# Performance work log

Hardware: AMD Instinct MI355X
Metric: run time of the kernel (lower is better)

## Reference

```python
import jax, jax.numpy as jnp
import numpy as np

M = 5            # Anderson memory
LAM = 1e-4       # Tikhonov regularization on Gram matrix
MAX_ITER = 50
TOL = 0.01
BETA = 1.0
BSZ, DIM = 64, 4096


def f_layer(z, x, W, b):
    # canonical DEQ cell: contraction so the fixed point exists
    return jnp.tanh(z @ W + x + b)


def anderson(f, x0, m=M, lam=LAM, max_iter=MAX_ITER, tol=TOL, beta=BETA):
    """Anderson acceleration; faithful port of DEQFixedPoint.anderson.
    Variable history length n=min(k,m) is handled by masking so the whole
    loop is jit-compatible (lax.while_loop with early stop on tol)."""
    bsz = x0.shape[0]
    d = int(np.prod(x0.shape[1:]))
    ff = lambda v: f(v.reshape(x0.shape)).reshape(bsz, d)
    x0f = x0.reshape(bsz, d)

    X = jnp.zeros((bsz, m, d), x0.dtype)
    F = jnp.zeros((bsz, m, d), x0.dtype)
    F0 = ff(x0f)
    F1 = ff(F0)
    X = X.at[:, 0].set(x0f).at[:, 1].set(F0)
    F = F.at[:, 0].set(F0).at[:, 1].set(F1)

    y = jnp.zeros((bsz, m + 1, 1), x0.dtype).at[:, 0, 0].set(1.0)
    eye_m = jnp.eye(m, dtype=x0.dtype)

    def cond(state):
        _, _, k, res = state
        return (k < max_iter) & (res >= tol)

    def body(state):
        X, F, k, res = state
        n = jnp.minimum(k, m)
        mask = (jnp.arange(m) < n).astype(x0.dtype)          # active history slots
        G = (F - X) * mask[None, :, None]                     # (bsz, m, d)
        GG = jnp.einsum('bmd,bnd->bmn', G, G)                 # small 5x5 Gram
        # masked (n+1)x(n+1) subproblem embedded in (m+1)x(m+1): inactive
        # rows become identity rows with zero rhs -> alpha_i = 0 for i >= n,
        # exactly matching torch's solve on the leading (n+1) block.
        Hin = (GG + lam * eye_m) * (mask[:, None] * mask[None, :]) + jnp.diag(1.0 - mask)
        H = jnp.zeros((bsz, m + 1, m + 1), x0.dtype)
        H = H.at[:, 0, 1:].set(mask).at[:, 1:, 0].set(mask).at[:, 1:, 1:].set(Hin)
        alpha = jnp.linalg.solve(H, y)[:, 1:, 0]              # (bsz, m)
        Xk = beta * jnp.einsum('bm,bmd->bd', alpha, F) + (1.0 - beta) * jnp.einsum('bm,bmd->bd', alpha, X)
        Fk = ff(Xk)
        idx = k % m
        Xn = X.at[:, idx].set(Xk)
        Fn = F.at[:, idx].set(Fk)
        r = jnp.linalg.norm(Fk - Xk) / (1e-5 + jnp.linalg.norm(Fk))
        return Xn, Fn, k + 1, r

    init = (X, F, jnp.array(2, jnp.int32), jnp.array(jnp.inf, x0.dtype))
    X, F, k, res = jax.lax.while_loop(cond, body, init)
    idx = (k - 1) % m  # k was incremented after the last executed iteration
    return X[:, idx].reshape(x0.shape)


def setup_inputs():
    key = jax.random.key(0)
    kx, kw, kb = jax.random.split(key, 3)
    x = jax.random.normal(kx, (BSZ, DIM), jnp.float32)
    # spectral norm of W ~ 2 * 0.4 = 0.8 -> contraction through tanh
    W = jax.random.normal(kw, (DIM, DIM), jnp.float32) * (0.4 / np.sqrt(DIM))
    b = jax.random.normal(kb, (DIM,), jnp.float32) * 0.1
    return {"x": x, "W": W, "b": b}


def reference(x, W, b):
    # forward: solve z* = f(z*, x) with no grad, then one grad-carrying f step
    zstar = anderson(lambda z: f_layer(z, x, W, b), jnp.zeros_like(x))
    return f_layer(zstar, x, W, b)
```

## Files before the change

### kernel.cpp

```cpp
#include <hip/hip_runtime.h>

#define NBLK 256
#define GBLK 128
#define NTHR 1024
#define BSZ 64
#define DIM 4096
#define MEM 5
#define MAXIT 50
#define TOL_ 0.01f
#define LAM_ 1e-4f

#define X_OFF 0
#define F_OFF (BSZ * MEM * DIM)
#define Z_OFF (2 * BSZ * MEM * DIM)
#define RP_OFF (Z_OFF + BSZ * DIM)
#define BAR_OFF (RP_OFF + 512)
#define FP32_WS_FLOATS (RP_OFF + 1024)
#define ZF_BYTE ((size_t)(RP_OFF + 1024) * 4)
#define WF_BYTE (ZF_BYTE + (size_t)BSZ * DIM * 2)
#define WS_NEED (WF_BYTE + (size_t)DIM * DIM * 2)

typedef __attribute__((ext_vector_type(8))) _Float16 half8v;
typedef __attribute__((ext_vector_type(4))) float f32x4;

__device__ __forceinline__ unsigned short f2h(float f) {
    _Float16 h = (_Float16)f;
    unsigned short u;
    __builtin_memcpy(&u, &h, 2);
    return u;
}

__device__ __forceinline__ void gridbar(unsigned int* flags, unsigned int* go,
                                        unsigned int e)
{
    __syncthreads();
    const int tid = threadIdx.x;
    if (blockIdx.x == 0) {
        if (tid == 0) {
            __builtin_amdgcn_fence(__ATOMIC_RELEASE, "agent");
            __hip_atomic_store(&flags[0], e, __ATOMIC_RELAXED,
                               __HIP_MEMORY_SCOPE_AGENT);
        }
        if (tid < NBLK) {
            while (__hip_atomic_load(&flags[tid], __ATOMIC_RELAXED,
                                     __HIP_MEMORY_SCOPE_AGENT) < e)
                __builtin_amdgcn_s_sleep(1);
        }
        __syncthreads();
        if (tid == 0)
            __builtin_amdgcn_fence(__ATOMIC_ACQUIRE, "agent");
        __syncthreads();
        if (tid < 8)
            __hip_atomic_store(&go[tid << 5], e, __ATOMIC_RELAXED,
                               __HIP_MEMORY_SCOPE_AGENT);
    } else {
        if (tid == 0) {
            __builtin_amdgcn_fence(__ATOMIC_RELEASE, "agent");
            __hip_atomic_store(&flags[blockIdx.x], e, __ATOMIC_RELAXED,
                               __HIP_MEMORY_SCOPE_AGENT);
            while (__hip_atomic_load(&go[(blockIdx.x >> 5) << 5], __ATOMIC_RELAXED,
                                     __HIP_MEMORY_SCOPE_AGENT) < e)
                __builtin_amdgcn_s_sleep(1);
            __builtin_amdgcn_fence(__ATOMIC_ACQUIRE, "agent");
        }
    }
    __syncthreads();
}

__device__ void convert_w(const float* __restrict__ W, unsigned short* __restrict__ Wf,
                          float* smem)
{
    const int tid = threadIdx.x;
    const int blk = blockIdx.x;
    const int jc = blk << 4;
    for (int sc = 0; sc < 8; ++sc) {
        __syncthreads();
        #pragma unroll
        for (int h = 0; h < 2; ++h) {
            int rrow = (tid >> 2) + (h << 8);
            int seg = tid & 3;
            float4 v = *(const float4*)&W[(size_t)((sc << 9) + rrow) * DIM + jc + (seg << 2)];
            float* dst = smem + rrow * 17 + (seg << 2);
            dst[0] = v.x; dst[1] = v.y; dst[2] = v.z; dst[3] = v.w;
        }
        __syncthreads();
        unsigned int* of = (unsigned int*)(Wf + ((size_t)blk * 128 + sc * 16) * 512);
        #pragma unroll
        for (int it = 0; it < 4; ++it) {
            int o = tid + (it << 10);
            int ksl = o >> 8, ln = (o >> 2) & 63, ep = o & 3;
            int kl = (ksl << 5) + ((ln >> 4) << 3) + (ep << 1);
            float w0 = smem[kl * 17 + (ln & 15)];
            float w1 = smem[(kl + 1) * 17 + (ln & 15)];
            of[o] = (unsigned int)f2h(w0) | ((unsigned int)f2h(w1) << 16);
        }
    }
    __syncthreads();
}

__device__ __forceinline__ void gemm_tanh_mfma(
    int idx, const float* __restrict__ x, const float* __restrict__ bias,
    const unsigned short* __restrict__ Zf, const unsigned short* __restrict__ Wf,
    float* __restrict__ Z, float* __restrict__ Fs, float* __restrict__ rp, float* smem)
{
    const int tid = threadIdx.x;
    const int cb = blockIdx.x;
    const int lane = tid & 63;
    const int w = tid >> 6;
    const int r0 = lane & 15;
    const int kg = lane >> 4;
    f32x4 acc[4][2] = {};

    const unsigned short* b0 = Wf + (size_t)(cb * 2) * 65536;
    const unsigned short* b1 = Wf + (size_t)(cb * 2 + 1) * 65536;
    const int ksbase = w << 3;

    #pragma unroll 2
    for (int s = 0; s < 8; ++s) {
        const int ks = ksbase + s;
        const size_t bo = ((size_t)ks << 9) + (lane << 3);
        half8v B0 = *(const half8v*)(b0 + bo);
        half8v B1 = *(const half8v*)(b1 + bo);
        const int kbase = (ks << 5) + (kg << 3);
        #pragma unroll
        for (int m = 0; m < 4; ++m) {
            const size_t ao = (size_t)((m << 4) + r0) * DIM + kbase;
            half8v Ah = *(const half8v*)(Zf + ao);
            acc[m][0] = __builtin_amdgcn_mfma_f32_16x16x32_f16(Ah, B0, acc[m][0], 0, 0, 0);
            acc[m][1] = __builtin_amdgcn_mfma_f32_16x16x32_f16(Ah, B1, acc[m][1], 0, 0, 0);
        }
    }
    const int row = tid >> 4, cc = tid & 15;
    const int m_o = row >> 4, rl = row & 15;
    const int lsrc = cc + ((rl >> 2) << 4), reg = rl & 3;
    float sum0 = 0.f, sum1 = 0.f;
    #pragma unroll
    for (int rnd = 0; rnd < 4; ++rnd) {
        __syncthreads();
        if ((w >> 2) == rnd) {
            float* sec = smem + (w & 3) * 2052;
            #pragma unroll
            for (int m = 0; m < 4; ++m) {
                *(f32x4*)(sec + ((m * 2 + 0) << 8) + (lane << 2)) = acc[m][0];
                *(f32x4*)(sec + ((m * 2 + 1) << 8) + (lane << 2)) = acc[m][1];
            }
        }
        __syncthreads();
        #pragma unroll
        for (int p = 0; p < 4; ++p) {
            sum0 += smem[p * 2052 + ((m_o * 2 + 0) << 8) + (lsrc << 2) + reg];
            sum1 += smem[p * 2052 + ((m_o * 2 + 1) << 8) + (lsrc << 2) + reg];
        }
    }
    const int j0 = (cb << 5) + cc;
    const int j1 = j0 + 16;
    float fz0 = tanhf(sum0 + x[(row << 12) + j0] + bias[j0]);
    float fz1 = tanhf(sum1 + x[(row << 12) + j1] + bias[j1]);
    Fs[(row * MEM + idx) * DIM + j0] = fz0;
    Fs[(row * MEM + idx) * DIM + j1] = fz1;
    float d0 = fz0 - Z[(row << 12) + j0];
    float d1 = fz1 - Z[(row << 12) + j1];
    float lnum = d0 * d0 + d1 * d1;
    float lden = fz0 * fz0 + fz1 * fz1;
    #pragma unroll
    for (int off = 1; off < 64; off <<= 1) {
        lnum += __shfl_xor(lnum, off, 64);
        lden += __shfl_xor(lden, off, 64);
    }
    if (lane == 0) { smem[8448 + w] = lnum; smem[8480 + w] = lden; }
    __syncthreads();
    if (tid == 0) {
        float a = 0.f, b2 = 0.f;
        #pragma unroll
        for (int i = 0; i < 16; ++i) { a += smem[8448 + i]; b2 += smem[8480 + i]; }
        rp[cb] = a;
        rp[NBLK + cb] = b2;
    }
}

__device__ __forceinline__ void gemm_tanh_fp32(
    int idx, const float* __restrict__ x, const float* __restrict__ W,
    const float* __restrict__ bias, float* __restrict__ wsf, float* smem)
{
    const int tid = threadIdx.x;
    const int blk = blockIdx.x;
    const int lane = tid & 63;
    const int w = tid >> 6;
    const int r = w >> 2;
    const int q = w & 3;
    const int jcq = (blk << 4) + (q << 2);
    float* Z = wsf + Z_OFF;
    float* Fs = wsf + F_OFF;
    float* rp = wsf + RP_OFF;

    float acc0 = 0.f, acc1 = 0.f, acc2 = 0.f, acc3 = 0.f;
    const int lx = lane & 15;
    const float* inrow = smem + (r << 12) + (lane << 6);
    const int srow = tid >> 4;
    const int sg = tid & 15;

    for (int step = 0; step < 16; ++step) {
        #pragma unroll
        for (int i = 0; i < 4; ++i) {
            float4 v = *(const float4*)&Z[srow * DIM + (i << 10) + (step << 6) + (sg << 2)];
            *(float4*)&smem[(i << 12) + (srow << 6) + ((sg ^ (srow & 15)) << 2)] = v;
        }
        __syncthreads();
        const float* wbase = W + (size_t)((r << 10) + (step << 6)) * DIM + jcq;
        #pragma unroll 2
        for (int s = 0; s < 16; ++s) {
            float4 in4 = *(const float4*)&inrow[(s ^ lx) << 2];
            const float* wr = wbase + (size_t)(s << 2) * DIM;
            #pragma unroll
            for (int t = 0; t < 4; ++t) {
                float iv = (t == 0) ? in4.x : (t == 1) ? in4.y : (t == 2) ? in4.z : in4.w;
                float4 wq = *(const float4*)(wr + (size_t)t * DIM);
                acc0 = fmaf(iv, wq.x, acc0);
                acc1 = fmaf(iv, wq.y, acc1);
                acc2 = fmaf(iv, wq.z, acc2);
                acc3 = fmaf(iv, wq.w, acc3);
            }
        }
        __syncthreads();
    }
    {
        float* rrow = smem + r * 1088 + lane * 17 + (q << 2);
        rrow[0] = acc0; rrow[1] = acc1; rrow[2] = acc2; rrow[3] = acc3;
    }
    __syncthreads();
    const int row = tid >> 4, cc = tid & 15;
    const int boff = row * 17 + cc;
    float sum = smem[boff] + smem[1088 + boff] + smem[2176 + boff] + smem[3264 + boff];
    const int j = (blk << 4) + cc;
    float fz = tanhf(sum + x[(row << 12) + j] + bias[j]);
    Fs[(row * MEM + idx) * DIM + j] = fz;
    float d = fz - Z[(row << 12) + j];
    float lnum = d * d, lden = fz * fz;
    #pragma unroll
    for (int off = 1; off < 64; off <<= 1) {
        lnum += __shfl_xor(lnum, off, 64);
        lden += __shfl_xor(lden, off, 64);
    }
    if (lane == 0) { smem[8448 + w] = lnum; smem[8480 + w] = lden; }
    __syncthreads();
    if (tid == 0) {
        float a = 0.f, b2 = 0.f;
        for (int i = 0; i < 16; ++i) { a += smem[8448 + i]; b2 += smem[8480 + i]; }
        rp[blk] = a;
        rp[NBLK + blk] = b2;
    }
}

__device__ __forceinline__ float phase_res(const float* __restrict__ rp, float* smem)
{
    const int tid = threadIdx.x;
    const int lane = tid & 63, w = tid >> 6;
    float a = (tid < NBLK) ? rp[tid] : 0.f;
    float b = (tid < NBLK) ? rp[NBLK + tid] : 0.f;
    #pragma unroll
    for (int off = 1; off < 64; off <<= 1) {
        a += __shfl_xor(a, off, 64);
        b += __shfl_xor(b, off, 64);
    }
    if (lane == 0) { smem[w] = a; smem[16 + w] = b; }
    __syncthreads();
    if (tid == 0) {
        float sa = 0.f, sb = 0.f;
        for (int i = 0; i < 16; ++i) { sa += smem[i]; sb += smem[16 + i]; }
        smem[32] = sqrtf(sa) / (1e-5f + sqrtf(sb));
    }
    __syncthreads();
    float res = smem[32];
    __syncthreads();
    return res;
}

template <bool F16>
__device__ void gram_solve_combine(int b, int n, int idx, float* __restrict__ wsf,
                                   unsigned short* __restrict__ Zf, float* smem)
{
    const int tid = threadIdx.x;
    const int lane = tid & 63, w = tid >> 6;
    float* Xs = wsf + X_OFF;
    float* Fs = wsf + F_OFF;
    float* Z = wsf + Z_OFF;
    const int j4 = tid << 2;

    float fv[MEM][4];
    float g[MEM][4];
    #pragma unroll
    for (int i = 0; i < MEM; ++i) {
        float4 f4 = *(const float4*)&Fs[(b * MEM + i) * DIM + j4];
        float4 xv = *(const float4*)&Xs[(b * MEM + i) * DIM + j4];
        fv[i][0] = f4.x; fv[i][1] = f4.y; fv[i][2] = f4.z; fv[i][3] = f4.w;
        bool act = (i < n);
        g[i][0] = act ? (f4.x - xv.x) : 0.f;
        g[i][1] = act ? (f4.y - xv.y) : 0.f;
        g[i][2] = act ? (f4.z - xv.z) : 0.f;
        g[i][3] = act ? (f4.w - xv.w) : 0.f;
    }
    float gg[15];
    {
        int p = 0;
        #pragma unroll
        for (int i = 0; i < MEM; ++i)
            #pragma unroll
            for (int qq = i; qq < MEM; ++qq) {
                float s = 0.f;
                #pragma unroll
                for (int c = 0; c < 4; ++c) s = fmaf(g[i][c], g[qq][c], s);
                gg[p++] = s;
            }
    }
    #pragma unroll
    for (int off = 1; off < 64; off <<= 1)
        #pragma unroll
        for (int p = 0; p < 15; ++p) gg[p] += __shfl_xor(gg[p], off, 64);
    if (lane == 0) {
        #pragma unroll
        for (int p = 0; p < 15; ++p) smem[p * 16 + w] = gg[p];
    }
    __syncthreads();
    if (tid == 0) {
        float G[MEM][MEM];
        int p = 0;
        for (int i = 0; i < MEM; ++i)
            for (int qq = i; qq < MEM; ++qq) {
                float v = 0.f;
                for (int ww = 0; ww < 16; ++ww) v += smem[p * 16 + ww];
                G[i][qq] = v; G[qq][i] = v; ++p;
            }
        float H[6][6], yv[6];
        for (int i = 0; i < 6; ++i) yv[i] = (i == 0) ? 1.f : 0.f;
        H[0][0] = 0.f;
        for (int i = 0; i < MEM; ++i) {
            float mi = (i < n) ? 1.f : 0.f;
            H[0][1 + i] = mi;
            H[1 + i][0] = mi;
        }
        for (int i = 0; i < MEM; ++i)
            for (int qq = 0; qq < MEM; ++qq) {
                float v;
                if (i < n && qq < n) v = G[i][qq] + ((i == qq) ? LAM_ : 0.f);
                else v = (i == qq) ? 1.f : 0.f;
                H[1 + i][1 + qq] = v;
            }
        for (int col = 0; col < 6; ++col) {
            int piv = col;
            float mv = fabsf(H[col][col]);
            for (int rr = col + 1; rr < 6; ++rr) {
                float av = fabsf(H[rr][col]);
                if (av > mv) { mv = av; piv = rr; }
            }
            if (piv != col) {
                for (int c2 = 0; c2 < 6; ++c2) { float tv = H[col][c2]; H[col][c2] = H[piv][c2]; H[piv][c2] = tv; }
                float tv = yv[col]; yv[col] = yv[piv]; yv[piv] = tv;
            }
            float pv = H[col][col];
            for (int rr = col + 1; rr < 6; ++rr) {
                float f = H[rr][col] / pv;
                H[rr][col] = 0.f;
                for (int c2 = col + 1; c2 < 6; ++c2) H[rr][c2] -= f * H[col][c2];
                yv[rr] -= f * yv[col];
            }
        }
        float sol[6];
        for (int col = 5; col >= 0; --col) {
            float s = yv[col];
            for (int c2 = col + 1; c2 < 6; ++c2) s -= H[col][c2] * sol[c2];
            sol[col] = s / H[col][col];
        }
        for (int i = 0; i < MEM; ++i) smem[240 + i] = sol[1 + i];
    }
    __syncthreads();
    float al[MEM];
    #pragma unroll
    for (int i = 0; i < MEM; ++i) al[i] = smem[240 + i];
    float4 zf = {0.f, 0.f, 0.f, 0.f};
    #pragma unroll
    for (int i = 0; i < MEM; ++i) {
        zf.x = fmaf(al[i], fv[i][0], zf.x);
        zf.y = fmaf(al[i], fv[i][1], zf.y);
        zf.z = fmaf(al[i], fv[i][2], zf.z);
        zf.w = fmaf(al[i], fv[i][3], zf.w);
    }
    *(float4*)&Z[(b << 12) + j4] = zf;
    *(float4*)&Xs[(b * MEM + idx) * DIM + j4] = zf;
    if constexpr (F16) {
        unsigned int* z16 = (unsigned int*)(Zf + ((size_t)b << 12) + j4);
        z16[0] = (unsigned int)f2h(zf.x) | ((unsigned int)f2h(zf.y) << 16);
        z16[1] = (unsigned int)f2h(zf.z) | ((unsigned int)f2h(zf.w) << 16);
    }
}

template <bool F16>
__global__ __launch_bounds__(NTHR, 4)
void deq_anderson(const float* __restrict__ x, const float* __restrict__ W,
                  const float* __restrict__ bias, float* __restrict__ out,
                  char* __restrict__ ws)
{
    __shared__ __align__(16) float smem[16384];
    float* wsf = (float*)ws;
    unsigned int* flags = (unsigned int*)(wsf + BAR_OFF);
    unsigned int* go = flags + 256;
    unsigned short* Zf = (unsigned short*)(ws + ZF_BYTE);
    unsigned short* Wf = (unsigned short*)(ws + WF_BYTE);
    const int tid = threadIdx.x;
    const int blk = blockIdx.x;
    const int e = blk * NTHR + tid;
    const int b = e >> 12, j = e & (DIM - 1);
    float* Xs = wsf + X_OFF;
    float* Fs = wsf + F_OFF;
    float* Z = wsf + Z_OFF;
    float* rp = wsf + RP_OFF;
    unsigned int ep = 1;

    {
        float f0 = tanhf(x[e] + bias[j]);
        #pragma unroll
        for (int i = 0; i < MEM; ++i) {
            Xs[(b * MEM + i) * DIM + j] = (i == 1) ? f0 : 0.f;
            Fs[(b * MEM + i) * DIM + j] = (i == 0) ? f0 : 0.f;
        }
        Z[e] = f0;
        if constexpr (F16) Zf[e] = f2h(f0);
    }
    if constexpr (F16) convert_w(W, Wf, smem);
    gridbar(flags, go, ep++);
    if constexpr (F16) {
        if (blk < GBLK)
            gemm_tanh_mfma(1, x, bias, Zf, Wf, Z, Fs, rp, smem);
        else if (tid == 0) { rp[blk] = 0.f; rp[NBLK + blk] = 0.f; }
    } else {
        gemm_tanh_fp32(1, x, W, bias, wsf, smem);
    }
    gridbar(flags, go, ep++);

    int kend = MAXIT;
    for (int k = 2; k < MAXIT; ++k) {
        float res = phase_res(rp, smem);
        if (k > 2 && res < TOL_) { kend = k; break; }
        const int n = (k < MEM) ? k : MEM;
        const int idx = k % MEM;
        if (blk < BSZ) gram_solve_combine<F16>(blk, n, idx, wsf, Zf, smem);
        gridbar(flags, go, ep++);
        if constexpr (F16) {
            if (blk < GBLK)
                gemm_tanh_mfma(idx, x, bias, Zf, Wf, Z, Fs, rp, smem);
        } else {
            gemm_tanh_fp32(idx, x, W, bias, wsf, smem);
        }
        gridbar(flags, go, ep++);
    }

    const int fidx = (kend - 1) % MEM;
    out[e] = Fs[(b * MEM + fidx) * DIM + j];
}

extern "C" void kernel_launch(void* const* d_in, const int* in_sizes, int n_in,
                              void* d_out, int out_size, void* d_ws, size_t ws_size,
                              hipStream_t stream)
{
    (void)in_sizes; (void)n_in; (void)out_size;
    if (ws_size < (size_t)FP32_WS_FLOATS * sizeof(float)) return;
    const float* x = (const float*)d_in[0];
    const float* W = (const float*)d_in[1];
    const float* b = (const float*)d_in[2];
    float* out = (float*)d_out;
    char* ws = (char*)d_ws;
    hipMemsetAsync(ws + (size_t)BAR_OFF * 4, 0, 2048, stream);
    void* args[] = {(void*)&x, (void*)&W, (void*)&b, (void*)&out, (void*)&ws};
    const void* fn = (ws_size >= WS_NEED)
                         ? reinterpret_cast<const void*>(&deq_anderson<true>)
                         : reinterpret_cast<const void*>(&deq_anderson<false>);
    hipLaunchCooperativeKernel(fn, dim3(NBLK), dim3(NTHR), args, 0, stream);
}
```

Measured before the change: 245.4 us.

## Prefetch first W tile before grid barrier and simplify barrier release flag

The first k-slice of the fp16 W tiles is now loaded into registers before the grid barrier that precedes each GEMM, so that load overlaps the barrier wait. The grid barrier release also changes from eight spread-out go flags written after an extra __syncthreads to a single go word written by thread 0, which removes one block-level sync on the master block. In exchange, all 255 blocks now poll the same address, which can increase contention on that cache line. The barrier buffer layout and memset size are adjusted to match.

```diff
diff --git a/kernel.cpp b/kernel.cpp
--- a/kernel.cpp
+++ b/kernel.cpp
@@ -14,7 +14,7 @@
 #define F_OFF (BSZ * MEM * DIM)
 #define Z_OFF (2 * BSZ * MEM * DIM)
 #define RP_OFF (Z_OFF + BSZ * DIM)
-#define BAR_OFF (RP_OFF + 512)
+#define BAR_OFF (RP_OFF + 640)
 #define FP32_WS_FLOATS (RP_OFF + 1024)
 #define ZF_BYTE ((size_t)(RP_OFF + 1024) * 4)
 #define WF_BYTE (ZF_BYTE + (size_t)BSZ * DIM * 2)
@@ -47,18 +47,17 @@
                 __builtin_amdgcn_s_sleep(1);
         }
         __syncthreads();
-        if (tid == 0)
+        if (tid == 0) {
             __builtin_amdgcn_fence(__ATOMIC_ACQUIRE, "agent");
-        __syncthreads();
-        if (tid < 8)
-            __hip_atomic_store(&go[tid << 5], e, __ATOMIC_RELAXED,
+            __hip_atomic_store(go, e, __ATOMIC_RELAXED,
                                __HIP_MEMORY_SCOPE_AGENT);
+        }
     } else {
         if (tid == 0) {
             __builtin_amdgcn_fence(__ATOMIC_RELEASE, "agent");
             __hip_atomic_store(&flags[blockIdx.x], e, __ATOMIC_RELAXED,
                                __HIP_MEMORY_SCOPE_AGENT);
-            while (__hip_atomic_load(&go[(blockIdx.x >> 5) << 5], __ATOMIC_RELAXED,
+            while (__hip_atomic_load(go, __ATOMIC_RELAXED,
                                      __HIP_MEMORY_SCOPE_AGENT) < e)
                 __builtin_amdgcn_s_sleep(1);
             __builtin_amdgcn_fence(__ATOMIC_ACQUIRE, "agent");
@@ -98,10 +97,12 @@
     __syncthreads();
 }
 
+template <bool PRE>
 __device__ __forceinline__ void gemm_tanh_mfma(
     int idx, const float* __restrict__ x, const float* __restrict__ bias,
     const unsigned short* __restrict__ Zf, const unsigned short* __restrict__ Wf,
-    float* __restrict__ Z, float* __restrict__ Fs, float* __restrict__ rp, float* smem)
+    float* __restrict__ Z, float* __restrict__ Fs, float* __restrict__ rp, float* smem,
+    unsigned int* flags, unsigned int* go, unsigned int ep)
 {
     const int tid = threadIdx.x;
     const int cb = blockIdx.x;
@@ -114,9 +115,31 @@
     const unsigned short* b0 = Wf + (size_t)(cb * 2) * 65536;
     const unsigned short* b1 = Wf + (size_t)(cb * 2 + 1) * 65536;
     const int ksbase = w << 3;
-
+    const size_t bo0 = ((size_t)ksbase << 9) + (lane << 3);
+
+    half8v B0p, B1p;
+    if constexpr (PRE) {
+        B0p = *(const half8v*)(b0 + bo0);
+        B1p = *(const half8v*)(b1 + bo0);
+        gridbar(flags, go, ep);
+    } else {
+        gridbar(flags, go, ep);
+        B0p = *(const half8v*)(b0 + bo0);
+        B1p = *(const half8v*)(b1 + bo0);
+    }
+
+    {
+        const int kbase = (ksbase << 5) + (kg << 3);
+        #pragma unroll
+        for (int m = 0; m < 4; ++m) {
+            const size_t ao = (size_t)((m << 4) + r0) * DIM + kbase;
+            half8v Ah = *(const half8v*)(Zf + ao);
+            acc[m][0] = __builtin_amdgcn_mfma_f32_16x16x32_f16(Ah, B0p, acc[m][0], 0, 0, 0);
+            acc[m][1] = __builtin_amdgcn_mfma_f32_16x16x32_f16(Ah, B1p, acc[m][1], 0, 0, 0);
+        }
+    }
     #pragma unroll 2
-    for (int s = 0; s < 8; ++s) {
+    for (int s = 1; s < 8; ++s) {
         const int ks = ksbase + s;
         const size_t bo = ((size_t)ks << 9) + (lane << 3);
         half8v B0 = *(const half8v*)(b0 + bo);
@@ -402,7 +425,7 @@
     __shared__ __align__(16) float smem[16384];
     float* wsf = (float*)ws;
     unsigned int* flags = (unsigned int*)(wsf + BAR_OFF);
-    unsigned int* go = flags + 256;
+    unsigned int* go = flags + 272;
     unsigned short* Zf = (unsigned short*)(ws + ZF_BYTE);
     unsigned short* Wf = (unsigned short*)(ws + WF_BYTE);
     const int tid = threadIdx.x;
@@ -425,13 +448,17 @@
         Z[e] = f0;
         if constexpr (F16) Zf[e] = f2h(f0);
     }
-    if constexpr (F16) convert_w(W, Wf, smem);
-    gridbar(flags, go, ep++);
     if constexpr (F16) {
-        if (blk < GBLK)
-            gemm_tanh_mfma(1, x, bias, Zf, Wf, Z, Fs, rp, smem);
-        else if (tid == 0) { rp[blk] = 0.f; rp[NBLK + blk] = 0.f; }
+        convert_w(W, Wf, smem);
+        if (blk < GBLK) {
+            gemm_tanh_mfma<false>(1, x, bias, Zf, Wf, Z, Fs, rp, smem, flags, go, ep);
+        } else {
+            gridbar(flags, go, ep);
+            if (tid == 0) { rp[blk] = 0.f; rp[NBLK + blk] = 0.f; }
+        }
+        ++ep;
     } else {
+        gridbar(flags, go, ep++);
         gemm_tanh_fp32(1, x, W, bias, wsf, smem);
     }
     gridbar(flags, go, ep++);
@@ -443,11 +470,14 @@
         const int n = (k < MEM) ? k : MEM;
         const int idx = k % MEM;
         if (blk < BSZ) gram_solve_combine<F16>(blk, n, idx, wsf, Zf, smem);
-        gridbar(flags, go, ep++);
         if constexpr (F16) {
             if (blk < GBLK)
-                gemm_tanh_mfma(idx, x, bias, Zf, Wf, Z, Fs, rp, smem);
+                gemm_tanh_mfma<true>(idx, x, bias, Zf, Wf, Z, Fs, rp, smem, flags, go, ep);
+            else
+                gridbar(flags, go, ep);
+            ++ep;
         } else {
+            gridbar(flags, go, ep++);
             gemm_tanh_fp32(idx, x, W, bias, wsf, smem);
         }
         gridbar(flags, go, ep++);
@@ -468,7 +498,7 @@
     const float* b = (const float*)d_in[2];
     float* out = (float*)d_out;
     char* ws = (char*)d_ws;
-    hipMemsetAsync(ws + (size_t)BAR_OFF * 4, 0, 2048, stream);
+    hipMemsetAsync(ws + (size_t)BAR_OFF * 4, 0, 1152, stream);
     void* args[] = {(void*)&x, (void*)&W, (void*)&b, (void*)&out, (void*)&ws};
     const void* fn = (ws_size >= WS_NEED)
                          ? reinterpret_cast<const void*>(&deq_anderson<true>)
```

Measured after the change: 286.8 us. +16.9%, slower.
